# Kernel tuning notes

Measured on AMD Instinct MI355X. Metric: run time of the kernel, lower is better.

The kernel has to match this reference:

```python
import jax, jax.numpy as jnp
import numpy as np

NUM_UNITS = 32   # nodes per graph (obs_dim 160 / 5)
B = 2048         # graphs per batch
FEAT_IN = 5
NUM_OUT = 5


def setup_inputs() -> dict:
    key = jax.random.key(0)
    ks = jax.random.split(key, 16)
    obs = jax.random.normal(ks[0], (B, NUM_UNITS * FEAT_IN), dtype=jnp.float32)
    # Fully-connected (incl. self-loop) edge list per graph, offset by graph id.
    i = jnp.arange(NUM_UNITS, dtype=jnp.int32)
    s, d = jnp.meshgrid(i, i, indexing='ij')          # all 32x32 pairs
    offs = (jnp.arange(B, dtype=jnp.int32) * NUM_UNITS)[:, None]
    src = (s.reshape(-1)[None, :] + offs).reshape(-1)  # [B*1024]
    dst = (d.reshape(-1)[None, :] + offs).reshape(-1)
    def lin(k, fin, fout):
        return jax.random.normal(k, (fout, fin), dtype=jnp.float32) * (1.0 / np.sqrt(fin))
    return {
        'obs': obs, 'src': src, 'dst': dst,
        'W1l': lin(ks[1], 5, 64),  'b1': jnp.zeros((64,), jnp.float32),  'W1r': lin(ks[2], 5, 64),
        'W2l': lin(ks[3], 64, 128), 'b2': jnp.zeros((128,), jnp.float32), 'W2r': lin(ks[4], 64, 128),
        'W3l': lin(ks[5], 128, 128), 'b3': jnp.zeros((128,), jnp.float32), 'W3r': lin(ks[6], 128, 128),
        'Wp': lin(ks[7], 128, NUM_OUT), 'bp': jnp.zeros((NUM_OUT,), jnp.float32),
    }


def reference(obs, src, dst, W1l, b1, W1r, W2l, b2, W2r, W3l, b3, W3r, Wp, bp):
    x = obs.reshape(-1, FEAT_IN)                 # [N, 5], N = B*32
    N = x.shape[0]
    deg = jnp.float32(NUM_UNITS)                 # every node has 32 in-edges

    def sage(h, Wl, b, Wr):
        # PyG SAGEConv: lin_l(mean_{j->i} h_j) + lin_r(h_i); bias lives in lin_l
        msg = h[src]                             # gather  [E, F]
        agg = jax.ops.segment_sum(msg, dst, num_segments=N) / deg
        return agg @ Wl.T + b + h @ Wr.T

    h = jax.nn.relu(sage(x, W1l, b1, W1r))
    h = jax.nn.relu(sage(h, W2l, b2, W2r))
    h = jax.nn.relu(sage(h, W3l, b3, W3r))
    pooled = h.reshape(B, NUM_UNITS, 128).mean(axis=1)   # global_mean_pool (equal-size graphs)
    return pooled @ Wp.T + bp                    # policy_out [B, NUM_OUT]
```

## Files before the change

### kernel.cpp

```cpp
#include <hip/hip_runtime.h>
#include <hip/hip_bf16.h>


typedef float f32x4 __attribute__((ext_vector_type(4)));
typedef __bf16 bf16x8 __attribute__((ext_vector_type(8)));

__device__ __forceinline__ f32x4 MFMA(bf16x8 a, bf16x8 b, f32x4 c) {
  return __builtin_amdgcn_mfma_f32_16x16x32_bf16(a, b, c, 0, 0, 0);
}

__device__ __forceinline__ unsigned short bfbits(float v) {
  __hip_bfloat16 t = __float2bfloat16(v);
  return __builtin_bit_cast(unsigned short, t);
}

__device__ __forceinline__ bf16x8 pack8(f32x4 lo, f32x4 hi) {
  union { bf16x8 v; unsigned short u[8]; } t;
  t.u[0] = bfbits(lo[0]); t.u[1] = bfbits(lo[1]);
  t.u[2] = bfbits(lo[2]); t.u[3] = bfbits(lo[3]);
  t.u[4] = bfbits(hi[0]); t.u[5] = bfbits(hi[1]);
  t.u[6] = bfbits(hi[2]); t.u[7] = bfbits(hi[3]);
  return t.v;
}

__device__ __forceinline__ void packmat(const float* __restrict__ W,
                                        unsigned short* __restrict__ dst,
                                        int KB, int Kreal, int tid) {
  const int iters = (128 * KB) / 512;
#pragma unroll
  for (int it = 0; it < 4; ++it) {
    if (it >= iters) break;
    int tau = it * 512 + tid;
    int f = tau & 127, kb = tau >> 7;
    const float* srcp = W + f * Kreal + kb * 8;
    f32x4 lo = *(const f32x4*)(srcp);
    f32x4 hi = *(const f32x4*)(srcp + 4);
    int ks = kb >> 2, gg = kb & 3;
    int fragbase = (((f >> 4) * (KB >> 2) + ks) * 64 + gg * 16 + (f & 15)) * 8;
    *(bf16x8*)(dst + fragbase) = pack8(lo, hi);
  }
}

__device__ __forceinline__ void qpass(float* rb, float* mb, int lane, int fbase,
                                      f32x4 t00, f32x4 t01, f32x4 t10, f32x4 t11,
                                      bf16x8* Bn0, bf16x8* Bn1, bf16x8* Bg) {
  const int g = lane >> 4, c = lane & 15;
  *(f32x4*)(rb + c * 36 + 4 * g)             = t00;
  *(f32x4*)(rb + c * 36 + 16 + 4 * g)        = t01;
  *(f32x4*)(rb + (16 + c) * 36 + 4 * g)      = t10;
  *(f32x4*)(rb + (16 + c) * 36 + 16 + 4 * g) = t11;
  const int qd = lane & 7, rg = lane >> 3;
  f32x4 s = {0.f, 0.f, 0.f, 0.f};
#pragma unroll
  for (int rr = 0; rr < 4; ++rr)
    s += *(const f32x4*)(rb + (rg * 4 + rr) * 36 + qd * 4);
#pragma unroll
  for (int i = 0; i < 4; ++i) {
    float v = s[i];
    v += __shfl_xor(v, 8, 64); v += __shfl_xor(v, 16, 64); v += __shfl_xor(v, 32, 64);
    s[i] = v * 0.03125f;
  }
  if (lane < 8) *(f32x4*)(mb + fbase + qd * 4) = s;
  if (Bn0) {
    f32x4 lo0 = *(const f32x4*)(rb + c * 36 + 8 * g);
    f32x4 hi0 = *(const f32x4*)(rb + c * 36 + 8 * g + 4);
    *Bn0 = pack8(lo0, hi0);
    f32x4 lo1 = *(const f32x4*)(rb + (16 + c) * 36 + 8 * g);
    f32x4 hi1 = *(const f32x4*)(rb + (16 + c) * 36 + 8 * g + 4);
    *Bn1 = pack8(lo1, hi1);
    f32x4 glo = *(const f32x4*)(mb + fbase + 8 * g);
    f32x4 ghi = *(const f32x4*)(mb + fbase + 8 * g + 4);
    *Bg = pack8(glo, ghi);
  }
}

__global__ __launch_bounds__(512) void gnn_fused(
    const float* __restrict__ obs,
    const float* __restrict__ W1l, const float* __restrict__ W1r,
    const float* __restrict__ W2l, const float* __restrict__ W2r,
    const float* __restrict__ W3l, const float* __restrict__ W3r,
    const float* __restrict__ b1, const float* __restrict__ b2,
    const float* __restrict__ b3,
    const float* __restrict__ Wp, const float* __restrict__ bp,
    float* __restrict__ out)
{
  __shared__ unsigned short smA2[16384];
  __shared__ unsigned short smA3[32768];
  __shared__ float rb_all[8][32 * 36];
  __shared__ float mb_all[8][128];

  const int tid  = threadIdx.x;
  const int wid  = tid >> 6;
  const int lane = tid & 63;
  const int g    = lane >> 4;
  const int c    = lane & 15;
  float* rb = &rb_all[wid][0];
  float* mb = &mb_all[wid][0];
  const int graph = blockIdx.x * 8 + wid;
  const float* xg = obs + graph * 160;

  packmat(W2r, smA2,         8,  64, tid);
  packmat(W2l, smA2 + 8192,  8,  64, tid);
  packmat(W3r, smA3,         16, 128, tid);
  packmat(W3l, smA3 + 16384, 16, 128, tid);

  const f32x4 Z4 = {0.f, 0.f, 0.f, 0.f};

  bf16x8 ar1[4], al1[4];
#pragma unroll
  for (int ft = 0; ft < 4; ++ft) {
    float wr[5], wl[5];
#pragma unroll
    for (int j = 0; j < 5; ++j) {
      wr[j] = (g == 0) ? W1r[(ft * 16 + c) * 5 + j] : 0.f;
      wl[j] = (g == 0) ? W1l[(ft * 16 + c) * 5 + j] : 0.f;
    }
    f32x4 rlo = {wr[0], wr[1], wr[2], wr[3]}, rhi = {wr[4], 0.f, 0.f, 0.f};
    f32x4 llo = {wl[0], wl[1], wl[2], wl[3]}, lhi = {wl[4], 0.f, 0.f, 0.f};
    ar1[ft] = pack8(rlo, rhi);
    al1[ft] = pack8(llo, lhi);
  }

  float x0[5], x1[5];
#pragma unroll
  for (int j = 0; j < 5; ++j) { x0[j] = xg[c * 5 + j]; x1[j] = xg[80 + c * 5 + j]; }
  float m0[5];
#pragma unroll
  for (int j = 0; j < 5; ++j) {
    float s = x0[j] + x1[j];
    s += __shfl_xor(s, 1, 64); s += __shfl_xor(s, 2, 64);
    s += __shfl_xor(s, 4, 64); s += __shfl_xor(s, 8, 64);
    m0[j] = s * 0.03125f;
  }
  bf16x8 Bn1[2], Bg1;
  {
    f32x4 a0 = {x0[0], x0[1], x0[2], x0[3]}, a1 = {x0[4], 0.f, 0.f, 0.f};
    f32x4 n0 = {x1[0], x1[1], x1[2], x1[3]}, n1 = {x1[4], 0.f, 0.f, 0.f};
    f32x4 g0 = {m0[0], m0[1], m0[2], m0[3]}, g1 = {m0[4], 0.f, 0.f, 0.f};
    if (g != 0) { a0 = Z4; a1 = Z4; n0 = Z4; n1 = Z4; g0 = Z4; g1 = Z4; }
    Bn1[0] = pack8(a0, a1); Bn1[1] = pack8(n0, n1); Bg1 = pack8(g0, g1);
  }

  f32x4 acc[2][8];
#pragma unroll
  for (int ft = 0; ft < 4; ++ft) {
    f32x4 bias = *(const f32x4*)(b1 + ft * 16 + 4 * g);
    acc[0][ft] = bias; acc[1][ft] = bias;
    acc[0][ft] = MFMA(ar1[ft], Bn1[0], acc[0][ft]);
    acc[1][ft] = MFMA(ar1[ft], Bn1[1], acc[1][ft]);
    acc[0][ft] = MFMA(al1[ft], Bg1, acc[0][ft]);
    acc[1][ft] = MFMA(al1[ft], Bg1, acc[1][ft]);
  }
#pragma unroll
  for (int ct = 0; ct < 2; ++ct)
#pragma unroll
    for (int ft = 0; ft < 4; ++ft)
#pragma unroll
      for (int i = 0; i < 4; ++i)
        acc[ct][ft][i] = fmaxf(acc[ct][ft][i], 0.f);

  bf16x8 Bn2[2][2], Bg2[2];
  qpass(rb, mb, lane, 0,  acc[0][0], acc[0][1], acc[1][0], acc[1][1],
        &Bn2[0][0], &Bn2[1][0], &Bg2[0]);
  qpass(rb, mb, lane, 32, acc[0][2], acc[0][3], acc[1][2], acc[1][3],
        &Bn2[0][1], &Bn2[1][1], &Bg2[1]);

  __syncthreads();

  {
    const unsigned short* A2r = smA2;
    const unsigned short* A2l = smA2 + 8192;
#pragma unroll
    for (int ft = 0; ft < 8; ++ft) {
      f32x4 bias = *(const f32x4*)(b2 + ft * 16 + 4 * g);
      acc[0][ft] = bias; acc[1][ft] = bias;
#pragma unroll
      for (int ks = 0; ks < 2; ++ks) {
        bf16x8 ar = *(const bf16x8*)(A2r + ((ft * 2 + ks) * 64 + lane) * 8);
        bf16x8 al = *(const bf16x8*)(A2l + ((ft * 2 + ks) * 64 + lane) * 8);
        acc[0][ft] = MFMA(ar, Bn2[0][ks], acc[0][ft]);
        acc[1][ft] = MFMA(ar, Bn2[1][ks], acc[1][ft]);
        acc[0][ft] = MFMA(al, Bg2[ks], acc[0][ft]);
        acc[1][ft] = MFMA(al, Bg2[ks], acc[1][ft]);
      }
    }
  }
#pragma unroll
  for (int ct = 0; ct < 2; ++ct)
#pragma unroll
    for (int ft = 0; ft < 8; ++ft)
#pragma unroll
      for (int i = 0; i < 4; ++i)
        acc[ct][ft][i] = fmaxf(acc[ct][ft][i], 0.f);

  bf16x8 Bn3[2][4], Bg3[4];
#pragma unroll
  for (int ks = 0; ks < 4; ++ks)
    qpass(rb, mb, lane, 32 * ks,
          acc[0][2 * ks], acc[0][2 * ks + 1], acc[1][2 * ks], acc[1][2 * ks + 1],
          &Bn3[0][ks], &Bn3[1][ks], &Bg3[ks]);

  {
    const unsigned short* A3r = smA3;
    const unsigned short* A3l = smA3 + 16384;
#pragma unroll
    for (int ft = 0; ft < 8; ++ft) {
      f32x4 bias = *(const f32x4*)(b3 + ft * 16 + 4 * g);
      acc[0][ft] = bias; acc[1][ft] = bias;
#pragma unroll
      for (int ks = 0; ks < 4; ++ks) {
        bf16x8 ar = *(const bf16x8*)(A3r + ((ft * 4 + ks) * 64 + lane) * 8);
        bf16x8 al = *(const bf16x8*)(A3l + ((ft * 4 + ks) * 64 + lane) * 8);
        acc[0][ft] = MFMA(ar, Bn3[0][ks], acc[0][ft]);
        acc[1][ft] = MFMA(ar, Bn3[1][ks], acc[1][ft]);
        acc[0][ft] = MFMA(al, Bg3[ks], acc[0][ft]);
        acc[1][ft] = MFMA(al, Bg3[ks], acc[1][ft]);
      }
    }
  }
#pragma unroll
  for (int ct = 0; ct < 2; ++ct)
#pragma unroll
    for (int ft = 0; ft < 8; ++ft)
#pragma unroll
      for (int i = 0; i < 4; ++i)
        acc[ct][ft][i] = fmaxf(acc[ct][ft][i], 0.f);

#pragma unroll
  for (int ks = 0; ks < 4; ++ks)
    qpass(rb, mb, lane, 32 * ks,
          acc[0][2 * ks], acc[0][2 * ks + 1], acc[1][2 * ks], acc[1][2 * ks + 1],
          nullptr, nullptr, nullptr);

  float p0 = mb[lane], p1 = mb[64 + lane];
  float po[5];
#pragma unroll
  for (int o = 0; o < 5; ++o)
    po[o] = p0 * Wp[o * 128 + lane] + p1 * Wp[o * 128 + 64 + lane];
#pragma unroll
  for (int o = 0; o < 5; ++o) {
    float v = po[o];
    v += __shfl_xor(v, 1, 64);  v += __shfl_xor(v, 2, 64);
    v += __shfl_xor(v, 4, 64);  v += __shfl_xor(v, 8, 64);
    v += __shfl_xor(v, 16, 64); v += __shfl_xor(v, 32, 64);
    po[o] = v;
  }
  if (lane == 0) {
#pragma unroll
    for (int o = 0; o < 5; ++o) out[graph * 5 + o] = po[o] + bp[o];
  }
}

extern "C" void kernel_launch(void* const* d_in, const int* in_sizes, int n_in,
                              void* d_out, int out_size, void* d_ws, size_t ws_size,
                              hipStream_t stream)
{
  const float* obs = (const float*)d_in[0];
  const float* W1l = (const float*)d_in[3];
  const float* b1  = (const float*)d_in[4];
  const float* W1r = (const float*)d_in[5];
  const float* W2l = (const float*)d_in[6];
  const float* b2  = (const float*)d_in[7];
  const float* W2r = (const float*)d_in[8];
  const float* W3l = (const float*)d_in[9];
  const float* b3  = (const float*)d_in[10];
  const float* W3r = (const float*)d_in[11];
  const float* Wp  = (const float*)d_in[12];
  const float* bp  = (const float*)d_in[13];
  float* out = (float*)d_out;

  gnn_fused<<<256, 512, 0, stream>>>(obs, W1l, W1r, W2l, W2r, W3l, W3r,
                                     b1, b2, b3, Wp, bp, out);
}
```

Baseline: 24.79 us.

## Prepack weights to bf16 fragments in a prep kernel and DMA into LDS

Adds a separate prep kernel that converts all SAGE weight matrices into bf16 MFMA fragment layout in workspace once per call. The main kernel then copies the packed layer-2/3 weights straight into LDS with global_load_lds, overlapping the copy with layer-1 compute, and reads layer-1 fragments from global. The row stride of the per-wave reduction buffer changes from 36 to 37 floats to reduce LDS bank conflicts. This removes the per-block fp32 load and convert work on the weights but adds a second kernel launch and a dependency between the two kernels.

```diff
diff --git a/kernel.cpp b/kernel.cpp
--- a/kernel.cpp
+++ b/kernel.cpp
@@ -23,37 +23,44 @@
   return t.v;
 }
 
-__device__ __forceinline__ void packmat(const float* __restrict__ W,
-                                        unsigned short* __restrict__ dst,
-                                        int KB, int Kreal, int tid) {
-  const int iters = (128 * KB) / 512;
-#pragma unroll
-  for (int it = 0; it < 4; ++it) {
-    if (it >= iters) break;
-    int tau = it * 512 + tid;
-    int f = tau & 127, kb = tau >> 7;
-    const float* srcp = W + f * Kreal + kb * 8;
-    f32x4 lo = *(const f32x4*)(srcp);
-    f32x4 hi = *(const f32x4*)(srcp + 4);
-    int ks = kb >> 2, gg = kb & 3;
-    int fragbase = (((f >> 4) * (KB >> 2) + ks) * 64 + gg * 16 + (f & 15)) * 8;
-    *(bf16x8*)(dst + fragbase) = pack8(lo, hi);
-  }
-}
+__global__ __launch_bounds__(256) void gnn_prep(
+    const float* __restrict__ W1l, const float* __restrict__ W1r,
+    const float* __restrict__ W2l, const float* __restrict__ W2r,
+    const float* __restrict__ W3l, const float* __restrict__ W3r,
+    unsigned short* __restrict__ wpack)
+{
+  int e = blockIdx.x * 256 + threadIdx.x;
+  if (e >= 53248) return;
+  const float* src; int Kreal, KS, eloc;
+  if      (e < 2048)  { src = W1r; Kreal = 5;   KS = 1; eloc = e; }
+  else if (e < 4096)  { src = W1l; Kreal = 5;   KS = 1; eloc = e - 2048; }
+  else if (e < 12288) { src = W2r; Kreal = 64;  KS = 2; eloc = e - 4096; }
+  else if (e < 20480) { src = W2l; Kreal = 64;  KS = 2; eloc = e - 12288; }
+  else if (e < 36864) { src = W3r; Kreal = 128; KS = 4; eloc = e - 20480; }
+  else                { src = W3l; Kreal = 128; KS = 4; eloc = e - 36864; }
+  int j = eloc & 7, lane = (eloc >> 3) & 63, rest = eloc >> 9;
+  int ks = rest % KS, ft = rest / KS;
+  int f = ft * 16 + (lane & 15);
+  int k = ks * 32 + (lane >> 4) * 8 + j;
+  float v = (k < Kreal) ? src[f * Kreal + k] : 0.f;
+  wpack[e] = bfbits(v);
+}
+
+#define RBS 37
 
 __device__ __forceinline__ void qpass(float* rb, float* mb, int lane, int fbase,
                                       f32x4 t00, f32x4 t01, f32x4 t10, f32x4 t11,
                                       bf16x8* Bn0, bf16x8* Bn1, bf16x8* Bg) {
   const int g = lane >> 4, c = lane & 15;
-  *(f32x4*)(rb + c * 36 + 4 * g)             = t00;
-  *(f32x4*)(rb + c * 36 + 16 + 4 * g)        = t01;
-  *(f32x4*)(rb + (16 + c) * 36 + 4 * g)      = t10;
-  *(f32x4*)(rb + (16 + c) * 36 + 16 + 4 * g) = t11;
+  *(f32x4*)(rb + c * RBS + 4 * g)              = t00;
+  *(f32x4*)(rb + c * RBS + 16 + 4 * g)         = t01;
+  *(f32x4*)(rb + (16 + c) * RBS + 4 * g)       = t10;
+  *(f32x4*)(rb + (16 + c) * RBS + 16 + 4 * g)  = t11;
   const int qd = lane & 7, rg = lane >> 3;
   f32x4 s = {0.f, 0.f, 0.f, 0.f};
 #pragma unroll
   for (int rr = 0; rr < 4; ++rr)
-    s += *(const f32x4*)(rb + (rg * 4 + rr) * 36 + qd * 4);
+    s += *(const f32x4*)(rb + (rg * 4 + rr) * RBS + qd * 4);
 #pragma unroll
   for (int i = 0; i < 4; ++i) {
     float v = s[i];
@@ -62,11 +69,11 @@
   }
   if (lane < 8) *(f32x4*)(mb + fbase + qd * 4) = s;
   if (Bn0) {
-    f32x4 lo0 = *(const f32x4*)(rb + c * 36 + 8 * g);
-    f32x4 hi0 = *(const f32x4*)(rb + c * 36 + 8 * g + 4);
+    f32x4 lo0 = *(const f32x4*)(rb + c * RBS + 8 * g);
+    f32x4 hi0 = *(const f32x4*)(rb + c * RBS + 8 * g + 4);
     *Bn0 = pack8(lo0, hi0);
-    f32x4 lo1 = *(const f32x4*)(rb + (16 + c) * 36 + 8 * g);
-    f32x4 hi1 = *(const f32x4*)(rb + (16 + c) * 36 + 8 * g + 4);
+    f32x4 lo1 = *(const f32x4*)(rb + (16 + c) * RBS + 8 * g);
+    f32x4 hi1 = *(const f32x4*)(rb + (16 + c) * RBS + 8 * g + 4);
     *Bn1 = pack8(lo1, hi1);
     f32x4 glo = *(const f32x4*)(mb + fbase + 8 * g);
     f32x4 ghi = *(const f32x4*)(mb + fbase + 8 * g + 4);
@@ -76,17 +83,14 @@
 
 __global__ __launch_bounds__(512) void gnn_fused(
     const float* __restrict__ obs,
-    const float* __restrict__ W1l, const float* __restrict__ W1r,
-    const float* __restrict__ W2l, const float* __restrict__ W2r,
-    const float* __restrict__ W3l, const float* __restrict__ W3r,
     const float* __restrict__ b1, const float* __restrict__ b2,
     const float* __restrict__ b3,
     const float* __restrict__ Wp, const float* __restrict__ bp,
+    const unsigned short* __restrict__ wpack,
     float* __restrict__ out)
 {
-  __shared__ unsigned short smA2[16384];
-  __shared__ unsigned short smA3[32768];
-  __shared__ float rb_all[8][32 * 36];
+  __shared__ unsigned short smW[49152];
+  __shared__ float rb_all[8][32 * RBS];
   __shared__ float mb_all[8][128];
 
   const int tid  = threadIdx.x;
@@ -99,27 +103,23 @@
   const int graph = blockIdx.x * 8 + wid;
   const float* xg = obs + graph * 160;
 
-  packmat(W2r, smA2,         8,  64, tid);
-  packmat(W2l, smA2 + 8192,  8,  64, tid);
-  packmat(W3r, smA3,         16, 128, tid);
-  packmat(W3l, smA3 + 16384, 16, 128, tid);
+  const unsigned short* A1r = wpack;
+  const unsigned short* A1l = wpack + 2048;
+
+  {
+    const unsigned short* gW = wpack + 4096;
+#pragma unroll
+    for (int it = 0; it < 12; ++it) {
+      const int chunk = it * 8 + wid;
+      const void* gsrc = (const void*)((const char*)(gW + chunk * 512) + lane * 16);
+      __builtin_amdgcn_global_load_lds(
+          (const __attribute__((address_space(1))) unsigned int*)gsrc,
+          (__attribute__((address_space(3))) unsigned int*)&smW[chunk * 512],
+          16, 0, 0);
+    }
+  }
 
   const f32x4 Z4 = {0.f, 0.f, 0.f, 0.f};
-
-  bf16x8 ar1[4], al1[4];
-#pragma unroll
-  for (int ft = 0; ft < 4; ++ft) {
-    float wr[5], wl[5];
-#pragma unroll
-    for (int j = 0; j < 5; ++j) {
-      wr[j] = (g == 0) ? W1r[(ft * 16 + c) * 5 + j] : 0.f;
-      wl[j] = (g == 0) ? W1l[(ft * 16 + c) * 5 + j] : 0.f;
-    }
-    f32x4 rlo = {wr[0], wr[1], wr[2], wr[3]}, rhi = {wr[4], 0.f, 0.f, 0.f};
-    f32x4 llo = {wl[0], wl[1], wl[2], wl[3]}, lhi = {wl[4], 0.f, 0.f, 0.f};
-    ar1[ft] = pack8(rlo, rhi);
-    al1[ft] = pack8(llo, lhi);
-  }
 
   float x0[5], x1[5];
 #pragma unroll
@@ -146,10 +146,12 @@
   for (int ft = 0; ft < 4; ++ft) {
     f32x4 bias = *(const f32x4*)(b1 + ft * 16 + 4 * g);
     acc[0][ft] = bias; acc[1][ft] = bias;
-    acc[0][ft] = MFMA(ar1[ft], Bn1[0], acc[0][ft]);
-    acc[1][ft] = MFMA(ar1[ft], Bn1[1], acc[1][ft]);
-    acc[0][ft] = MFMA(al1[ft], Bg1, acc[0][ft]);
-    acc[1][ft] = MFMA(al1[ft], Bg1, acc[1][ft]);
+    bf16x8 ar = *(const bf16x8*)(A1r + (ft * 64 + lane) * 8);
+    bf16x8 al = *(const bf16x8*)(A1l + (ft * 64 + lane) * 8);
+    acc[0][ft] = MFMA(ar, Bn1[0], acc[0][ft]);
+    acc[1][ft] = MFMA(ar, Bn1[1], acc[1][ft]);
+    acc[0][ft] = MFMA(al, Bg1, acc[0][ft]);
+    acc[1][ft] = MFMA(al, Bg1, acc[1][ft]);
   }
 #pragma unroll
   for (int ct = 0; ct < 2; ++ct)
@@ -165,11 +167,12 @@
   qpass(rb, mb, lane, 32, acc[0][2], acc[0][3], acc[1][2], acc[1][3],
         &Bn2[0][1], &Bn2[1][1], &Bg2[1]);
 
+  asm volatile("s_waitcnt vmcnt(0)" ::: "memory");
   __syncthreads();
 
   {
-    const unsigned short* A2r = smA2;
-    const unsigned short* A2l = smA2 + 8192;
+    const unsigned short* A2r = smW;
+    const unsigned short* A2l = smW + 8192;
 #pragma unroll
     for (int ft = 0; ft < 8; ++ft) {
       f32x4 bias = *(const f32x4*)(b2 + ft * 16 + 4 * g);
@@ -201,8 +204,8 @@
           &Bn3[0][ks], &Bn3[1][ks], &Bg3[ks]);
 
   {
-    const unsigned short* A3r = smA3;
-    const unsigned short* A3l = smA3 + 16384;
+    const unsigned short* A3r = smW + 16384;
+    const unsigned short* A3l = smW + 32768;
 #pragma unroll
     for (int ft = 0; ft < 8; ++ft) {
       f32x4 bias = *(const f32x4*)(b3 + ft * 16 + 4 * g);
@@ -267,8 +270,9 @@
   const float* W3r = (const float*)d_in[11];
   const float* Wp  = (const float*)d_in[12];
   const float* bp  = (const float*)d_in[13];
+  unsigned short* wpack = (unsigned short*)d_ws;
   float* out = (float*)d_out;
 
-  gnn_fused<<<256, 512, 0, stream>>>(obs, W1l, W1r, W2l, W2r, W3l, W3r,
-                                     b1, b2, b3, Wp, bp, out);
-}
+  gnn_prep<<<208, 256, 0, stream>>>(W1l, W1r, W2l, W2r, W3l, W3r, wpack);
+  gnn_fused<<<256, 512, 0, stream>>>(obs, b1, b2, b3, Wp, bp, wpack, out);
+}
```

Measured after the change: 40.24 us. 1.62x slower.
